# Optimization experiments

Measured on AMD Instinct MI355X. Metric: run time of the kernel, lower is better.

The kernel has to match this reference:

```python
import jax, jax.numpy as jnp
import numpy as np

N = 50000   # nodes
E = 800000  # edges
D = 128     # hidden_dim
LN_EPS = 1e-5


def _mlp2(x, W1, b1, W2, b2, act_last):
    y = jax.nn.silu(x @ W1 + b1)
    y = y @ W2 + b2
    return jax.nn.silu(y) if act_last else y


def setup_inputs() -> dict:
    key = jax.random.key(0)
    ks = jax.random.split(key, 20)
    s = 1.0 / np.sqrt(D)
    inp = {
        "h": jax.random.normal(ks[0], (N, D), jnp.float32),
        "x": jax.random.normal(ks[1], (N, 3), jnp.float32),
        "vel_all": jax.random.normal(ks[2], (N, 5, 3), jnp.float32),
        "edge_index": jax.random.randint(ks[3], (2, E), 0, N, jnp.int64),
        # phi_e: Linear(2D+11, D) -> SiLU -> Linear(D, D) -> SiLU   (weights stored [in,out])
        "We1": jax.random.uniform(ks[4], (2 * D + 11, D), jnp.float32, -s, s),
        "be1": jax.random.uniform(ks[5], (D,), jnp.float32, -s, s),
        "We2": jax.random.uniform(ks[6], (D, D), jnp.float32, -s, s),
        "be2": jax.random.uniform(ks[7], (D,), jnp.float32, -s, s),
        # phi_x: Linear(D, D) -> SiLU -> Linear(D, 1)
        "Wx1": jax.random.uniform(ks[8], (D, D), jnp.float32, -s, s),
        "bx1": jax.random.uniform(ks[9], (D,), jnp.float32, -s, s),
        "Wx2": jax.random.uniform(ks[10], (D, 1), jnp.float32, -s, s),
        "bx2": jax.random.uniform(ks[11], (1,), jnp.float32, -s, s),
        # phi_h: Linear(2D, D) -> SiLU -> Linear(D, D)
        "Wh1": jax.random.uniform(ks[12], (2 * D, D), jnp.float32, -s, s),
        "bh1": jax.random.uniform(ks[13], (D,), jnp.float32, -s, s),
        "Wh2": jax.random.uniform(ks[14], (D, D), jnp.float32, -s, s),
        "bh2": jax.random.uniform(ks[15], (D,), jnp.float32, -s, s),
        # LayerNorm(D)
        "gamma": jnp.ones((D,), jnp.float32),
        "beta": jnp.zeros((D,), jnp.float32),
    }
    return inp


def reference(h, x, vel_all, edge_index, We1, be1, We2, be2, Wx1, bx1, Wx2, bx2,
              Wh1, bh1, Wh2, bh2, gamma, beta):
    n = h.shape[0]
    src, dst = edge_index[0], edge_index[1]

    rel = x[src] - x[dst]                                  # [E,3]
    dist2 = jnp.sum(rel * rel, axis=-1, keepdims=True)     # [E,1]
    dist = jnp.maximum(jnp.sqrt(dist2), 1e-8)
    r_hat = rel / dist                                     # [E,3]

    vel_proj_src = jnp.sum(vel_all[src] * r_hat[:, None, :], axis=-1)  # [E,5]
    vel_proj_dst = jnp.sum(vel_all[dst] * r_hat[:, None, :], axis=-1)  # [E,5]

    feat = jnp.concatenate([h[src], h[dst], dist2, vel_proj_src, vel_proj_dst], axis=-1)
    m_ij = _mlp2(feat, We1, be1, We2, be2, act_last=True)  # [E,D]

    # update_coords=True: scatter_mean of rel * phi_x(m_ij)
    coord_w = _mlp2(m_ij, Wx1, bx1, Wx2, bx2, act_last=False)          # [E,1]
    num = jax.ops.segment_sum(rel * coord_w, dst, num_segments=n)      # [N,3]
    cnt = jax.ops.segment_sum(jnp.ones((rel.shape[0], 1), x.dtype), dst, num_segments=n)
    delta_x = num / jnp.maximum(cnt, 1.0)
    x = x + delta_x

    agg = jax.ops.segment_sum(m_ij, dst, num_segments=n)               # [N,D]
    dh = _mlp2(jnp.concatenate([h, agg], axis=-1), Wh1, bh1, Wh2, bh2, act_last=False)
    h = h + dh  # dropout=0 -> identity

    # LayerNorm
    mu = jnp.mean(h, axis=-1, keepdims=True)
    var = jnp.mean(jnp.square(h - mu), axis=-1, keepdims=True)
    h = (h - mu) * jax.lax.rsqrt(var + LN_EPS) * gamma + beta

    return (h, x, m_ij)
```

## Files before the change

### kernel.cpp

```cpp
#include <hip/hip_runtime.h>
#include <stdint.h>

#define CAPB 64

typedef __attribute__((ext_vector_type(8))) short bf16x8;
typedef __attribute__((ext_vector_type(4))) float f32x4;

__device__ __forceinline__ float bf2f(unsigned short u){
  union { unsigned int i; float f; } v; v.i = ((unsigned int)u) << 16; return v.f;
}
__device__ __forceinline__ unsigned short f2bf(float f){
  union { float f; unsigned int i; } v; v.f = f;
  unsigned int x = v.i;
  unsigned int r = (x + 0x7FFFu + ((x >> 16) & 1u)) >> 16;
  return (unsigned short)r;
}
__device__ __forceinline__ float silu_f(float v){
  return v / (1.0f + __expf(-v));
}

template<bool F32> __device__ __forceinline__ float ldv(const void* p, size_t i){
  if (F32) return ((const float*)p)[i];
  return bf2f(((const unsigned short*)p)[i]);
}
template<bool F32> __device__ __forceinline__ void stv(void* p, size_t i, float v){
  if (F32) ((float*)p)[i] = v;
  else     ((unsigned short*)p)[i] = f2bf(v);
}
template<bool I64> __device__ __forceinline__ int ldidx(const int* p, size_t i){
  return I64 ? p[2*i] : p[i];
}

__global__ void detect_kernel(const unsigned int* gw, const int* eidx, int N, int* flags){
  int f = 0;
  if (gw[0] == 0x3F800000u) f |= 1;
  bool i64 = true;
  for (int k = 0; k < 4; k++){
    int lo = eidx[2*k], hi = eidx[2*k+1];
    if (hi != 0 || lo < 0 || lo >= N) i64 = false;
  }
  if (i64) f |= 2;
  flags[0] = f;
}

__global__ __launch_bounds__(256) void hist_kernel(
    const int* eidx, int* cnt_i, int* bucket, int* slot, int N, int E, const int* flags)
{
  int e = blockIdx.x * 256 + threadIdx.x;
  if (e >= E) return;
  int d;
  if (flags[0] & 2) d = eidx[2*((size_t)E + e)];
  else              d = eidx[(size_t)E + e];
  d = min(max(d, 0), N-1);
  int p = atomicAdd(&cnt_i[d], 1);
  slot[e] = p;
  if (p < CAPB) bucket[(size_t)d*CAPB + p] = e;
}

struct __align__(16) NodePreSmem { float hlt[128][36]; };

template<bool F32>
__device__ void node_pre_impl(NodePreSmem& S, const void* h, const void* We1,
                              unsigned short* H1a, unsigned short* H1b, int N)
{
  const int t = threadIdx.x;
  const int base = blockIdx.x * 32;
  for (int i = t; i < 32*128; i += 256){
    int nl = i >> 7, j = i & 127;
    int node = base + nl;
    S.hlt[j][nl] = (node < N) ? ldv<F32>(h, (size_t)node*128 + j) : 0.0f;
  }
  __syncthreads();
  const int j = t & 127, half = t >> 7;
  const size_t wbase = (size_t)(half * 128) * 128;
  unsigned short* O = half ? H1b : H1a;
  float acc[32];
  #pragma unroll
  for (int nl=0; nl<32; nl++) acc[nl] = 0.0f;
  #pragma unroll 2
  for (int k=0; k<128; k++){
    float w = ldv<F32>(We1, wbase + (size_t)k*128 + j);
    const float4* row = (const float4*)&S.hlt[k][0];
    #pragma unroll
    for (int g=0; g<8; g++){
      float4 hv = row[g];
      acc[g*4+0] += hv.x * w;
      acc[g*4+1] += hv.y * w;
      acc[g*4+2] += hv.z * w;
      acc[g*4+3] += hv.w * w;
    }
  }
  #pragma unroll
  for (int nl=0; nl<32; nl++){
    int node = base + nl;
    if (node < N) O[(size_t)node*128 + j] = f2bf(acc[nl]);
  }
}

__global__ __launch_bounds__(256) void node_pre(
    const void* h, const void* We1, unsigned short* H1a, unsigned short* H1b,
    int N, const int* flags)
{
  __shared__ NodePreSmem S;
  if (flags[0] & 1) node_pre_impl<true >(S, h, We1, H1a, H1b, N);
  else              node_pre_impl<false>(S, h, We1, H1a, H1b, N);
}

template<bool F32, bool I64, bool M1F32>
__device__ void m1_impl(
    const void* xu, const void* velu, const int* eidx,
    const unsigned short* __restrict__ H1a, const unsigned short* __restrict__ H1b,
    const void* We1, const void* be1,
    void* m1p, int N, int E)
{
  const int t = threadIdx.x;
  const int sub = t & 31;
  const int j0 = sub * 4;
  float gw[11][4];
  #pragma unroll
  for (int k=0;k<11;k++)
    #pragma unroll
    for (int c=0;c<4;c++) gw[k][c] = ldv<F32>(We1, (size_t)(256+k)*128 + j0 + c);
  float b1[4];
  #pragma unroll
  for (int c=0;c<4;c++) b1[c] = ldv<F32>(be1, j0 + c);

  int gid = blockIdx.x * 8 + (t >> 5);
  const int gstride = gridDim.x * 8;
  for (int e = gid; e < E; e += gstride){
    int s = ldidx<I64>(eidx, e);
    int d = ldidx<I64>(eidx, (size_t)E + e);
    s = min(max(s, 0), N-1);
    d = min(max(d, 0), N-1);
    float rx = ldv<F32>(xu,(size_t)s*3+0) - ldv<F32>(xu,(size_t)d*3+0);
    float ry = ldv<F32>(xu,(size_t)s*3+1) - ldv<F32>(xu,(size_t)d*3+1);
    float rz = ldv<F32>(xu,(size_t)s*3+2) - ldv<F32>(xu,(size_t)d*3+2);
    float dist2 = rx*rx + ry*ry + rz*rz;
    float dist = fmaxf(sqrtf(dist2), 1e-8f);
    float inv = 1.0f / dist;
    float ux = rx*inv, uy = ry*inv, uz = rz*inv;
    float geo[11];
    geo[0] = dist2;
    #pragma unroll
    for (int v=0; v<5; v++){
      geo[1+v] = ldv<F32>(velu,(size_t)s*15+v*3+0)*ux + ldv<F32>(velu,(size_t)s*15+v*3+1)*uy + ldv<F32>(velu,(size_t)s*15+v*3+2)*uz;
      geo[6+v] = ldv<F32>(velu,(size_t)d*15+v*3+0)*ux + ldv<F32>(velu,(size_t)d*15+v*3+1)*uy + ldv<F32>(velu,(size_t)d*15+v*3+2)*uz;
    }
    uint2 ua = *(const uint2*)&H1a[(size_t)s*128 + j0];
    uint2 ub = *(const uint2*)&H1b[(size_t)d*128 + j0];
    float a[4];
    a[0] = bf2f((unsigned short)(ua.x & 0xFFFFu)) + bf2f((unsigned short)(ub.x & 0xFFFFu)) + b1[0];
    a[1] = bf2f((unsigned short)(ua.x >> 16))     + bf2f((unsigned short)(ub.x >> 16))     + b1[1];
    a[2] = bf2f((unsigned short)(ua.y & 0xFFFFu)) + bf2f((unsigned short)(ub.y & 0xFFFFu)) + b1[2];
    a[3] = bf2f((unsigned short)(ua.y >> 16))     + bf2f((unsigned short)(ub.y >> 16))     + b1[3];
    #pragma unroll
    for (int k=0;k<11;k++){
      float g = geo[k];
      #pragma unroll
      for (int c=0;c<4;c++) a[c] += gw[k][c] * g;
    }
    #pragma unroll
    for (int c=0;c<4;c++) a[c] = silu_f(a[c]);
    if (M1F32){
      float4 v = { a[0], a[1], a[2], a[3] };
      *(float4*)((float*)m1p + (size_t)e*128 + j0) = v;
    } else {
      uint2 p;
      p.x = (unsigned int)f2bf(a[0]) | ((unsigned int)f2bf(a[1]) << 16);
      p.y = (unsigned int)f2bf(a[2]) | ((unsigned int)f2bf(a[3]) << 16);
      *(uint2*)((unsigned short*)m1p + (size_t)e*128 + j0) = p;
    }
  }
}

template<bool USE_WS>
__global__ __launch_bounds__(256) void m1_kernel(
    const void* xu, const void* velu, const int* eidx,
    const unsigned short* H1a, const unsigned short* H1b,
    const void* We1, const void* be1,
    void* m1ws, void* out, size_t moff, int N, int E, const int* flags)
{
  int f = flags[0];
  if (USE_WS){
    if      (f == 0) m1_impl<false,false,false>(xu,velu,eidx,H1a,H1b,We1,be1,m1ws,N,E);
    else if (f == 1) m1_impl<true ,false,false>(xu,velu,eidx,H1a,H1b,We1,be1,m1ws,N,E);
    else if (f == 2) m1_impl<false,true ,false>(xu,velu,eidx,H1a,H1b,We1,be1,m1ws,N,E);
    else             m1_impl<true ,true ,false>(xu,velu,eidx,H1a,H1b,We1,be1,m1ws,N,E);
  } else {
    if (f & 1){
      void* p = (void*)((float*)out + moff);
      if (f & 2) m1_impl<true,true ,true>(xu,velu,eidx,H1a,H1b,We1,be1,p,N,E);
      else       m1_impl<true,false,true>(xu,velu,eidx,H1a,H1b,We1,be1,p,N,E);
    } else {
      void* p = (void*)((unsigned short*)out + moff);
      if (f & 2) m1_impl<false,true ,false>(xu,velu,eidx,H1a,H1b,We1,be1,p,N,E);
      else       m1_impl<false,false,false>(xu,velu,eidx,H1a,H1b,We1,be1,p,N,E);
    }
  }
}

struct __align__(16) GemmSmem {
  unsigned short m1s[64][136];
  unsigned short m2s[64][136];
  float relv[192];
  int   dsts[64];
  int   slot[64];
  float wpart[4][64];
};

template<bool I64>
__device__ void gemm_async_impl(GemmSmem& S,
    const float* __restrict__ xu, const int* __restrict__ eidx,
    const unsigned short* __restrict__ m1p,
    const float* __restrict__ We2, const float* __restrict__ be2,
    const float* __restrict__ Wx1, const float* __restrict__ bx1,
    const float* __restrict__ Wx2, const float* __restrict__ bx2,
    float* __restrict__ out, size_t moff,
    float* __restrict__ agg, float* __restrict__ num,
    const int* __restrict__ slotp,
    int N, int E, int ntiles)
{
  const int t = threadIdx.x;
  const int wave = t >> 6, lane = t & 63;
  const int col = lane & 15, quad = lane >> 4;
  const int colbase = wave * 32;

  bf16x8 bwe2[2][4], bwx1[2][4];
  float wx2v[2], be2v[2], bx1v[2];
  #pragma unroll
  for (int nt=0; nt<2; nt++){
    int n = colbase + nt*16 + col;
    wx2v[nt] = Wx2[n]; be2v[nt] = be2[n]; bx1v[nt] = bx1[n];
    #pragma unroll
    for (int kb=0; kb<4; kb++){
      bf16x8 a, b;
      #pragma unroll
      for (int jj=0; jj<8; jj++){
        int k = kb*32 + quad*8 + jj;
        a[jj] = (short)f2bf(We2[(size_t)k*128 + n]);
        b[jj] = (short)f2bf(Wx1[(size_t)k*128 + n]);
      }
      bwe2[nt][kb] = a; bwx1[nt][kb] = b;
    }
  }
  const float bx2v = bx2[0];
  const int srow = t >> 2, sseg = t & 3;
  const int gs = gridDim.x;

  bf16x8 r0, r1, r2, r3;
  int nsv = 0, ndv = 0, nsl = 0;
  float prx = 0, pry = 0, prz = 0;
  int pdst = 0, pvalid = 0, have_w = 0;

  int tile = blockIdx.x;
  if (tile < ntiles){
    size_t e = (size_t)tile*64 + srow; if (e >= (size_t)E) e = (size_t)E - 1;
    const unsigned short* rp = m1p + e*128 + (size_t)sseg*32;
    r0 = *(const bf16x8*)(rp);      r1 = *(const bf16x8*)(rp + 8);
    r2 = *(const bf16x8*)(rp + 16); r3 = *(const bf16x8*)(rp + 24);
    if (t < 64){
      int ec = min(tile*64 + t, E-1);
      nsv = ldidx<I64>(eidx, ec);
      ndv = ldidx<I64>(eidx, (size_t)E + ec);
      nsl = slotp[ec];
    }
  }

  for (; tile < ntiles; tile += gs){
    const int ebase = tile * 64;
    if (t < 64){
      if (have_w && pvalid){
        float w = S.wpart[0][t] + S.wpart[1][t] + S.wpart[2][t] + S.wpart[3][t] + bx2v;
        atomicAdd(&num[(size_t)pdst*3+0], prx*w);
        atomicAdd(&num[(size_t)pdst*3+1], pry*w);
        atomicAdd(&num[(size_t)pdst*3+2], prz*w);
      }
      int s = min(max(nsv, 0), N-1), d = min(max(ndv, 0), N-1);
      S.dsts[t] = d; S.slot[t] = nsl;
      pvalid = (ebase + t) < E; pdst = d;
      prx = xu[(size_t)s*3+0] - xu[(size_t)d*3+0];
      pry = xu[(size_t)s*3+1] - xu[(size_t)d*3+1];
      prz = xu[(size_t)s*3+2] - xu[(size_t)d*3+2];
    }
    *(bf16x8*)&S.m1s[srow][sseg*32 +  0] = r0;
    *(bf16x8*)&S.m1s[srow][sseg*32 +  8] = r1;
    *(bf16x8*)&S.m1s[srow][sseg*32 + 16] = r2;
    *(bf16x8*)&S.m1s[srow][sseg*32 + 24] = r3;
    if (tile + gs < ntiles){
      size_t e = (size_t)(tile+gs)*64 + srow; if (e >= (size_t)E) e = (size_t)E - 1;
      const unsigned short* rp = m1p + e*128 + (size_t)sseg*32;
      r0 = *(const bf16x8*)(rp);      r1 = *(const bf16x8*)(rp + 8);
      r2 = *(const bf16x8*)(rp + 16); r3 = *(const bf16x8*)(rp + 24);
      if (t < 64){
        int ec = min((tile+gs)*64 + t, E-1);
        nsv = ldidx<I64>(eidx, ec);
        ndv = ldidx<I64>(eidx, (size_t)E + ec);
        nsl = slotp[ec];
      }
    }
    __syncthreads();
    const int erem = E - ebase;
    #pragma unroll
    for (int et=0; et<4; et++){
      #pragma unroll
      for (int nt=0; nt<2; nt++){
        f32x4 acc = { be2v[nt], be2v[nt], be2v[nt], be2v[nt] };
        #pragma unroll
        for (int kb=0; kb<4; kb++){
          bf16x8 a = *(const bf16x8*)&S.m1s[et*16 + col][kb*32 + quad*8];
          acc = __builtin_amdgcn_mfma_f32_16x16x32_bf16(a, bwe2[nt][kb], acc, 0, 0, 0);
        }
        int n = colbase + nt*16 + col;
        #pragma unroll
        for (int r=0; r<4; r++){
          int el = et*16 + quad*4 + r;
          float v = silu_f(acc[r]);
          S.m2s[el][n] = f2bf(v);
          if (el < erem){
            out[moff + (size_t)(ebase + el)*128 + n] = v;
            if (S.slot[el] >= CAPB)
              atomicAdd(&agg[(size_t)S.dsts[el]*128 + n], v);
          }
        }
      }
    }
    __syncthreads();
    float part[4][4];
    #pragma unroll
    for (int et=0; et<4; et++)
      #pragma unroll
      for (int r=0; r<4; r++) part[et][r] = 0.0f;
    #pragma unroll
    for (int et=0; et<4; et++){
      #pragma unroll
      for (int nt=0; nt<2; nt++){
        f32x4 acc = { bx1v[nt], bx1v[nt], bx1v[nt], bx1v[nt] };
        #pragma unroll
        for (int kb=0; kb<4; kb++){
          bf16x8 a = *(const bf16x8*)&S.m2s[et*16 + col][kb*32 + quad*8];
          acc = __builtin_amdgcn_mfma_f32_16x16x32_bf16(a, bwx1[nt][kb], acc, 0, 0, 0);
        }
        #pragma unroll
        for (int r=0; r<4; r++) part[et][r] += silu_f(acc[r]) * wx2v[nt];
      }
    }
    #pragma unroll
    for (int et=0; et<4; et++){
      #pragma unroll
      for (int r=0; r<4; r++){
        float v = part[et][r];
        v += __shfl_xor(v, 1, 16);
        v += __shfl_xor(v, 2, 16);
        v += __shfl_xor(v, 4, 16);
        v += __shfl_xor(v, 8, 16);
        part[et][r] = v;
      }
    }
    if (col == 0){
      #pragma unroll
      for (int et=0; et<4; et++)
        #pragma unroll
        for (int r=0; r<4; r++)
          S.wpart[wave][et*16 + quad*4 + r] = part[et][r];
    }
    __syncthreads();
    have_w = 1;
  }
  if (t < 64 && have_w && pvalid){
    float w = S.wpart[0][t] + S.wpart[1][t] + S.wpart[2][t] + S.wpart[3][t] + bx2v;
    atomicAdd(&num[(size_t)pdst*3+0], prx*w);
    atomicAdd(&num[(size_t)pdst*3+1], pry*w);
    atomicAdd(&num[(size_t)pdst*3+2], prz*w);
  }
}

template<bool F32, bool I64, bool M1F32>
__device__ void gemm_impl(GemmSmem& S,
    const void* xu, const int* eidx, const void* m1p,
    const void* We2, const void* be2, const void* Wx1, const void* bx1,
    const void* Wx2, const void* bx2,
    void* out, size_t moff,
    float* __restrict__ agg, float* __restrict__ num,
    const int* __restrict__ slotp,
    int N, int E, int ntiles)
{
  const int t = threadIdx.x;
  const int wave = t >> 6, lane = t & 63;
  const int col = lane & 15, quad = lane >> 4;
  const int colbase = wave * 32;

  bf16x8 bwe2[2][4], bwx1[2][4];
  float wx2v[2], be2v[2], bx1v[2];
  #pragma unroll
  for (int nt=0; nt<2; nt++){
    int n = colbase + nt*16 + col;
    wx2v[nt] = ldv<F32>(Wx2, n);
    be2v[nt] = ldv<F32>(be2, n);
    bx1v[nt] = ldv<F32>(bx1, n);
    #pragma unroll
    for (int kb=0; kb<4; kb++){
      bf16x8 a, b;
      #pragma unroll
      for (int jj=0; jj<8; jj++){
        int k = kb*32 + quad*8 + jj;
        a[jj] = (short)f2bf(ldv<F32>(We2, (size_t)k*128 + n));
        b[jj] = (short)f2bf(ldv<F32>(Wx1, (size_t)k*128 + n));
      }
      bwe2[nt][kb] = a; bwx1[nt][kb] = b;
    }
  }
  const int jfix = t & 127;
  const float bx2v = ldv<F32>(bx2, 0);
  const int srow = t >> 2, sseg = t & 3;

  for (int tile = blockIdx.x; tile < ntiles; tile += gridDim.x){
    const int ebase = tile * 64;
    {
      const int e = ebase + srow;
      if (M1F32){
        const float* rp = (const float*)m1p + (size_t)e*128 + sseg*32;
        #pragma unroll
        for (int q=0;q<4;q++){
          float4 va = {0,0,0,0}, vb = {0,0,0,0};
          if (e < E){ va = *(const float4*)(rp + q*8); vb = *(const float4*)(rp + q*8 + 4); }
          bf16x8 w;
          w[0]=(short)f2bf(va.x); w[1]=(short)f2bf(va.y); w[2]=(short)f2bf(va.z); w[3]=(short)f2bf(va.w);
          w[4]=(short)f2bf(vb.x); w[5]=(short)f2bf(vb.y); w[6]=(short)f2bf(vb.z); w[7]=(short)f2bf(vb.w);
          *(bf16x8*)&S.m1s[srow][sseg*32 + q*8] = w;
        }
      } else {
        const unsigned short* rp = (const unsigned short*)m1p + (size_t)e*128 + sseg*32;
        #pragma unroll
        for (int q=0;q<4;q++){
          bf16x8 w = {0,0,0,0,0,0,0,0};
          if (e < E) w = *(const bf16x8*)(rp + q*8);
          *(bf16x8*)&S.m1s[srow][sseg*32 + q*8] = w;
        }
      }
      if (t < 64){
        int e2 = ebase + t;
        int s2 = 0, d2 = 0, sl = 0;
        if (e2 < E){
          s2 = ldidx<I64>(eidx, e2);
          d2 = ldidx<I64>(eidx, (size_t)E + e2);
          sl = slotp[e2];
        }
        s2 = min(max(s2,0), N-1); d2 = min(max(d2,0), N-1);
        S.dsts[t] = d2; S.slot[t] = sl;
        S.relv[t*3+0] = ldv<F32>(xu,(size_t)s2*3+0) - ldv<F32>(xu,(size_t)d2*3+0);
        S.relv[t*3+1] = ldv<F32>(xu,(size_t)s2*3+1) - ldv<F32>(xu,(size_t)d2*3+1);
        S.relv[t*3+2] = ldv<F32>(xu,(size_t)s2*3+2) - ldv<F32>(xu,(size_t)d2*3+2);
      }
    }
    __syncthreads();
    #pragma unroll
    for (int et=0; et<4; et++){
      #pragma unroll
      for (int nt=0; nt<2; nt++){
        f32x4 acc = { be2v[nt], be2v[nt], be2v[nt], be2v[nt] };
        #pragma unroll
        for (int kb=0; kb<4; kb++){
          bf16x8 a = *(const bf16x8*)&S.m1s[et*16 + col][kb*32 + quad*8];
          acc = __builtin_amdgcn_mfma_f32_16x16x32_bf16(a, bwe2[nt][kb], acc, 0, 0, 0);
        }
        int n = colbase + nt*16 + col;
        #pragma unroll
        for (int r=0; r<4; r++)
          S.m2s[et*16 + quad*4 + r][n] = f2bf(silu_f(acc[r]));
      }
    }
    __syncthreads();
    if (F32){
      #pragma unroll
      for (int it=0; it<4; it++){
        const int sl = t + it*256;
        const int el = sl >> 4, i8 = sl & 15;
        const int e = ebase + el;
        if (e < E){
          const bf16x8 mv = *(const bf16x8*)&S.m2s[el][i8*8];
          float f[8];
          #pragma unroll
          for (int j=0; j<8; j++) f[j] = bf2f((unsigned short)mv[j]);
          float* op = (float*)out + moff + (size_t)e*128 + i8*8;
          float4 v0 = { f[0], f[1], f[2], f[3] };
          float4 v1 = { f[4], f[5], f[6], f[7] };
          *(float4*)op = v0;
          *(float4*)(op + 4) = v1;
          if (S.slot[el] >= CAPB){
            float* ap = &agg[(size_t)S.dsts[el]*128 + i8*8];
            #pragma unroll
            for (int j=0; j<8; j++) atomicAdd(ap + j, f[j]);
          }
        }
      }
    } else {
      #pragma unroll
      for (int it=0; it<32; it++){
        int el = (t + it*256) >> 7;
        int e = ebase + el;
        if (e < E){
          float v = bf2f(S.m2s[el][jfix]);
          stv<F32>(out, moff + (size_t)e*128 + jfix, v);
          atomicAdd(&agg[(size_t)S.dsts[el]*128 + jfix], v);
        }
      }
    }
    float part[4][4];
    #pragma unroll
    for (int et=0; et<4; et++)
      #pragma unroll
      for (int r=0; r<4; r++) part[et][r] = 0.0f;
    #pragma unroll
    for (int et=0; et<4; et++){
      #pragma unroll
      for (int nt=0; nt<2; nt++){
        f32x4 acc = { bx1v[nt], bx1v[nt], bx1v[nt], bx1v[nt] };
        #pragma unroll
        for (int kb=0; kb<4; kb++){
          bf16x8 a = *(const bf16x8*)&S.m2s[et*16 + col][kb*32 + quad*8];
          acc = __builtin_amdgcn_mfma_f32_16x16x32_bf16(a, bwx1[nt][kb], acc, 0, 0, 0);
        }
        #pragma unroll
        for (int r=0; r<4; r++) part[et][r] += silu_f(acc[r]) * wx2v[nt];
      }
    }
    #pragma unroll
    for (int et=0; et<4; et++){
      #pragma unroll
      for (int r=0; r<4; r++){
        float v = part[et][r];
        v += __shfl_xor(v, 1, 16);
        v += __shfl_xor(v, 2, 16);
        v += __shfl_xor(v, 4, 16);
        v += __shfl_xor(v, 8, 16);
        part[et][r] = v;
      }
    }
    if (col == 0){
      #pragma unroll
      for (int et=0; et<4; et++)
        #pragma unroll
        for (int r=0; r<4; r++)
          S.wpart[wave][et*16 + quad*4 + r] = part[et][r];
    }
    __syncthreads();
    if (t < 64){
      int e = ebase + t;
      if (e < E){
        float w = S.wpart[0][t] + S.wpart[1][t] + S.wpart[2][t] + S.wpart[3][t] + bx2v;
        int d = S.dsts[t];
        atomicAdd(&num[(size_t)d*3+0], S.relv[t*3+0]*w);
        atomicAdd(&num[(size_t)d*3+1], S.relv[t*3+1]*w);
        atomicAdd(&num[(size_t)d*3+2], S.relv[t*3+2]*w);
      }
    }
    __syncthreads();
  }
}

template<bool USE_WS>
__global__ __launch_bounds__(256) void gemm_kernel(
    const void* xu, const int* eidx, const void* m1ws,
    const void* We2, const void* be2, const void* Wx1, const void* bx1,
    const void* Wx2, const void* bx2,
    void* out, size_t moff, float* agg, float* num, const int* slotp,
    int N, int E, int ntiles, const int* flags)
{
  __shared__ GemmSmem S;
  int f = flags[0];
  if (USE_WS && (f & 1)){
    if (f & 2) gemm_async_impl<true >(S, (const float*)xu, eidx, (const unsigned short*)m1ws,
                                      (const float*)We2,(const float*)be2,(const float*)Wx1,(const float*)bx1,
                                      (const float*)Wx2,(const float*)bx2,
                                      (float*)out, moff, agg, num, slotp, N, E, ntiles);
    else       gemm_async_impl<false>(S, (const float*)xu, eidx, (const unsigned short*)m1ws,
                                      (const float*)We2,(const float*)be2,(const float*)Wx1,(const float*)bx1,
                                      (const float*)Wx2,(const float*)bx2,
                                      (float*)out, moff, agg, num, slotp, N, E, ntiles);
  } else if (USE_WS){
    if (f & 2) gemm_impl<false,true ,false>(S, xu, eidx, m1ws, We2,be2,Wx1,bx1,Wx2,bx2, out,moff, agg,num, slotp, N,E,ntiles);
    else       gemm_impl<false,false,false>(S, xu, eidx, m1ws, We2,be2,Wx1,bx1,Wx2,bx2, out,moff, agg,num, slotp, N,E,ntiles);
  } else {
    if (f & 1){
      const void* p = (const void*)((float*)out + moff);
      if (f & 2) gemm_impl<true,true ,true>(S, xu, eidx, p, We2,be2,Wx1,bx1,Wx2,bx2, out,moff, agg,num, slotp, N,E,ntiles);
      else       gemm_impl<true,false,true>(S, xu, eidx, p, We2,be2,Wx1,bx1,Wx2,bx2, out,moff, agg,num, slotp, N,E,ntiles);
    } else {
      const void* p = (const void*)((unsigned short*)out + moff);
      if (f & 2) gemm_impl<false,true ,false>(S, xu, eidx, p, We2,be2,Wx1,bx1,Wx2,bx2, out,moff, agg,num, slotp, N,E,ntiles);
      else       gemm_impl<false,false,false>(S, xu, eidx, p, We2,be2,Wx1,bx1,Wx2,bx2, out,moff, agg,num, slotp, N,E,ntiles);
    }
  }
}

struct __align__(16) NodeFinalSmem {
  unsigned short ins[16][256];
  unsigned short y1s[16][128];
  float hns[16][128];
};

template<bool F32>
__device__ void node_final_impl(NodeFinalSmem& S,
    const void* h, const void* xu,
    const float* __restrict__ agg, const float* __restrict__ num,
    const int* __restrict__ cnt_i, const int* __restrict__ bucket,
    const void* Wh1, const void* bh1, const void* Wh2, const void* bh2,
    const void* gam, const void* bet,
    void* out, size_t xoff, size_t moff, int N)
{
  const int t = threadIdx.x;
  const int base = blockIdx.x * 16;
  for (int i = t; i < 16*128; i += 256){
    int n = i >> 7, c = i & 127;
    int node = base + n;
    S.ins[n][c] = (node < N) ? f2bf(ldv<F32>(h, (size_t)node*128 + c)) : (unsigned short)0;
  }
  if (F32){
    const int g = t >> 4, i8 = t & 15;
    const int lanebase = (t & 63) & ~15;
    const int node = base + g;
    float a[8] = {0,0,0,0,0,0,0,0};
    if (node < N){
      int deg = cnt_i[node];
      int kmax = min(deg, CAPB);
      const float* mbase = (const float*)out + moff;
      for (int c0 = 0; c0 < kmax; c0 += 16){
        int ee = 0;
        if (c0 + i8 < kmax) ee = bucket[(size_t)node*CAPB + c0 + i8];
        int cnum = min(16, kmax - c0);
        #pragma unroll
        for (int k = 0; k < 16; k++){
          if (k < cnum){
            int e = __shfl(ee, lanebase + k, 64);
            const float* rp = mbase + (size_t)e*128 + i8*8;
            float4 v0 = *(const float4*)rp;
            float4 v1 = *(const float4*)(rp + 4);
            a[0]+=v0.x; a[1]+=v0.y; a[2]+=v0.z; a[3]+=v0.w;
            a[4]+=v1.x; a[5]+=v1.y; a[6]+=v1.z; a[7]+=v1.w;
          }
        }
      }
      if (deg > CAPB){
        const float* ap = &agg[(size_t)node*128 + i8*8];
        #pragma unroll
        for (int j=0; j<8; j++) a[j] += ap[j];
      }
    }
    #pragma unroll
    for (int j=0; j<8; j++) S.ins[g][128 + i8*8 + j] = f2bf(a[j]);
  } else {
    for (int i = t; i < 16*128; i += 256){
      int n = i >> 7, c = i & 127;
      int node = base + n;
      S.ins[n][128 + c] = (node < N) ? f2bf(agg[(size_t)node*128 + c]) : (unsigned short)0;
    }
  }
  __syncthreads();
  const int j = t & 127, nh = t >> 7;
  {
    float acc[8];
    #pragma unroll
    for (int u=0; u<8; u++) acc[u] = ldv<F32>(bh1, j);
    #pragma unroll 4
    for (int k=0; k<256; k++){
      float w = ldv<F32>(Wh1, (size_t)k*128 + j);
      #pragma unroll
      for (int u=0; u<8; u++) acc[u] += bf2f(S.ins[nh + 2*u][k]) * w;
    }
    #pragma unroll
    for (int u=0; u<8; u++) S.y1s[nh + 2*u][j] = f2bf(silu_f(acc[u]));
  }
  __syncthreads();
  {
    float acc[8];
    #pragma unroll
    for (int u=0; u<8; u++) acc[u] = ldv<F32>(bh2, j);
    #pragma unroll 4
    for (int k=0; k<128; k++){
      float w = ldv<F32>(Wh2, (size_t)k*128 + j);
      #pragma unroll
      for (int u=0; u<8; u++) acc[u] += bf2f(S.y1s[nh + 2*u][k]) * w;
    }
    #pragma unroll
    for (int u=0; u<8; u++){
      int n = nh + 2*u;
      int node = base + n;
      float hv = (node < N) ? ldv<F32>(h, (size_t)node*128 + j) : 0.0f;
      S.hns[n][j] = hv + acc[u];
    }
  }
  __syncthreads();
  {
    int n = t >> 4, sub = t & 15;
    float s = 0.0f, ss = 0.0f;
    #pragma unroll
    for (int i2=0; i2<8; i2++){
      float v = S.hns[n][sub + 16*i2];
      s += v; ss += v*v;
    }
    #pragma unroll
    for (int m=1; m<16; m<<=1){ s += __shfl_xor(s, m, 16); ss += __shfl_xor(ss, m, 16); }
    float mu = s * (1.0f/128.0f);
    float var = fmaxf(ss * (1.0f/128.0f) - mu*mu, 0.0f);
    float rs = rsqrtf(var + 1e-5f);
    int gnode = base + n;
    if (gnode < N){
      #pragma unroll
      for (int i2=0; i2<8; i2++){
        int jj = sub + 16*i2;
        float v = (S.hns[n][jj] - mu) * rs * ldv<F32>(gam, jj) + ldv<F32>(bet, jj);
        stv<F32>(out, (size_t)gnode*128 + jj, v);
      }
    }
  }
  if (t < 48){
    int n = t / 3, c = t % 3;
    int node = base + n;
    if (node < N){
      float cv = fmaxf((float)cnt_i[node], 1.0f);
      float dx = num[(size_t)node*3 + c] / cv;
      stv<F32>(out, xoff + (size_t)node*3 + c, ldv<F32>(xu, (size_t)node*3 + c) + dx);
    }
  }
}

__global__ __launch_bounds__(256) void node_final(
    const void* h, const void* xu,
    const float* agg, const float* num, const int* cnt_i, const int* bucket,
    const void* Wh1, const void* bh1, const void* Wh2, const void* bh2,
    const void* gam, const void* bet,
    void* out, size_t xoff, size_t moff, int N, const int* flags)
{
  __shared__ NodeFinalSmem S;
  if (flags[0] & 1) node_final_impl<true >(S, h, xu, agg, num, cnt_i, bucket, Wh1, bh1, Wh2, bh2, gam, bet, out, xoff, moff, N);
  else              node_final_impl<false>(S, h, xu, agg, num, cnt_i, bucket, Wh1, bh1, Wh2, bh2, gam, bet, out, xoff, moff, N);
}

extern "C" void kernel_launch(void* const* d_in, const int* in_sizes, int n_in,
                              void* d_out, int out_size, void* d_ws, size_t ws_size,
                              hipStream_t stream)
{
  const int N = in_sizes[0] / 128;
  const int E = in_sizes[3] / 2;

  char* ws = (char*)d_ws;
  int* flags = (int*)ws;
  size_t off = 256;
  unsigned short* H1a = (unsigned short*)(ws + off); off += (size_t)N*256;
  unsigned short* H1b = (unsigned short*)(ws + off); off += (size_t)N*256;
  float* agg   = (float*)(ws + off); off += (size_t)N*512;
  float* num   = (float*)(ws + off); off += (size_t)N*12;
  int*   cnt_i = (int*)(ws + off); off += (size_t)N*4;
  int*   bucket= (int*)(ws + off); off += (size_t)N*CAPB*4;
  int*   slot  = (int*)(ws + off); off += (size_t)E*4;
  void*  m1ws  = (void*)(ws + off); off += (size_t)E*256;
  const bool use_ws = (off <= ws_size);

  detect_kernel<<<1, 1, 0, stream>>>((const unsigned int*)d_in[16], (const int*)d_in[3], N, flags);

  size_t zbytes = (size_t)N*512 + (size_t)N*12 + (size_t)N*4;
  hipMemsetAsync((void*)agg, 0, zbytes, stream);

  hist_kernel<<<(E + 255) / 256, 256, 0, stream>>>((const int*)d_in[3], cnt_i, bucket, slot, N, E, flags);

  node_pre<<<(N + 31) / 32, 256, 0, stream>>>(d_in[0], d_in[4], H1a, H1b, N, flags);

  size_t xoff = (size_t)N * 128;
  size_t moff = (size_t)N * 128 + (size_t)N * 3;
  int ntiles = (E + 63) / 64;

  if (use_ws){
    m1_kernel<true><<<2048, 256, 0, stream>>>(d_in[1], d_in[2], (const int*)d_in[3], H1a, H1b,
                                              d_in[4], d_in[5], m1ws, d_out, moff, N, E, flags);
    gemm_kernel<true><<<2500, 256, 0, stream>>>(d_in[1], (const int*)d_in[3], m1ws,
                                                d_in[6], d_in[7], d_in[8], d_in[9],
                                                d_in[10], d_in[11],
                                                d_out, moff, agg, num, slot, N, E, ntiles, flags);
  } else {
    m1_kernel<false><<<2048, 256, 0, stream>>>(d_in[1], d_in[2], (const int*)d_in[3], H1a, H1b,
                                               d_in[4], d_in[5], m1ws, d_out, moff, N, E, flags);
    gemm_kernel<false><<<2500, 256, 0, stream>>>(d_in[1], (const int*)d_in[3], m1ws,
                                                 d_in[6], d_in[7], d_in[8], d_in[9],
                                                 d_in[10], d_in[11],
                                                 d_out, moff, agg, num, slot, N, E, ntiles, flags);
  }

  node_final<<<(N + 15) / 16, 256, 0, stream>>>(d_in[0], d_in[1], agg, num, cnt_i, bucket,
                                                d_in[12], d_in[13], d_in[14], d_in[15],
                                                d_in[16], d_in[17],
                                                d_out, xoff, moff, N, flags);
}
```

Before: 1.356 ms.

## Sort edges by destination via counting sort and segment-reduce aggregation in GEMM

Builds a destination-sorted edge permutation using histogram, a single-block prefix scan, and a scatter kernel. The edge MLP kernels then process edges in sorted order. The GEMM kernel reduces runs of equal destinations before issuing atomic adds to agg, and stores m_ij back to the original edge positions through the permutation. This removes the per-node bucket gather in the node kernel and the capped-bucket scheme. In exchange it adds extra launches including a serial single-block scan, scattered output writes, and the loss of the previous register prefetch pipeline in the GEMM kernel.

```diff
diff --git a/kernel.cpp b/kernel.cpp
--- a/kernel.cpp
+++ b/kernel.cpp
@@ -1,7 +1,5 @@
 #include <hip/hip_runtime.h>
 #include <stdint.h>
-
-#define CAPB 64
 
 typedef __attribute__((ext_vector_type(8))) short bf16x8;
 typedef __attribute__((ext_vector_type(4))) float f32x4;
@@ -44,7 +42,7 @@
 }
 
 __global__ __launch_bounds__(256) void hist_kernel(
-    const int* eidx, int* cnt_i, int* bucket, int* slot, int N, int E, const int* flags)
+    const int* eidx, int* cnt_i, int* slot, int N, int E, const int* flags)
 {
   int e = blockIdx.x * 256 + threadIdx.x;
   if (e >= E) return;
@@ -54,7 +52,47 @@
   d = min(max(d, 0), N-1);
   int p = atomicAdd(&cnt_i[d], 1);
   slot[e] = p;
-  if (p < CAPB) bucket[(size_t)d*CAPB + p] = e;
+}
+
+__global__ __launch_bounds__(256) void scan_kernel(const int* __restrict__ cnt_i, int* __restrict__ start, int N){
+  __shared__ int wsum[4];
+  const int t = threadIdx.x;
+  const int lane = t & 63, w = t >> 6;
+  int total = 0;
+  for (int base = 0; base < N; base += 256){
+    int i = base + t;
+    int v = (i < N) ? cnt_i[i] : 0;
+    int orig = v;
+    #pragma unroll
+    for (int off = 1; off < 64; off <<= 1){
+      int u = __shfl_up(v, off, 64);
+      if (lane >= off) v += u;
+    }
+    if (lane == 63) wsum[w] = v;
+    __syncthreads();
+    int wpre = 0;
+    #pragma unroll
+    for (int k = 0; k < 4; k++){
+      if (k < w) wpre += wsum[k];
+    }
+    int chunk_total = wsum[0] + wsum[1] + wsum[2] + wsum[3];
+    if (i < N) start[i] = total + wpre + (v - orig);
+    total += chunk_total;
+    __syncthreads();
+  }
+}
+
+__global__ __launch_bounds__(256) void perm_build(
+    const int* eidx, const int* slot, const int* start,
+    int* perm, int* dstp, int N, int E, const int* flags)
+{
+  int e = blockIdx.x * 256 + threadIdx.x;
+  if (e >= E) return;
+  int d = (flags[0] & 2) ? eidx[2*((size_t)E + e)] : eidx[(size_t)E + e];
+  d = min(max(d, 0), N-1);
+  int pos = start[d] + slot[e];
+  perm[pos] = e;
+  dstp[pos] = d;
 }
 
 struct __align__(16) NodePreSmem { float hlt[128][36]; };
@@ -106,12 +144,13 @@
   else              node_pre_impl<false>(S, h, We1, H1a, H1b, N);
 }
 
-template<bool F32, bool I64, bool M1F32>
+template<bool F32, bool I64, bool M1F32, bool PERM>
 __device__ void m1_impl(
     const void* xu, const void* velu, const int* eidx,
     const unsigned short* __restrict__ H1a, const unsigned short* __restrict__ H1b,
     const void* We1, const void* be1,
-    void* m1p, int N, int E)
+    void* m1p, const int* __restrict__ permp, float* __restrict__ relp,
+    int N, int E)
 {
   const int t = threadIdx.x;
   const int sub = t & 31;
@@ -127,7 +166,8 @@
 
   int gid = blockIdx.x * 8 + (t >> 5);
   const int gstride = gridDim.x * 8;
-  for (int e = gid; e < E; e += gstride){
+  for (int pos = gid; pos < E; pos += gstride){
+    const int e = PERM ? permp[pos] : pos;
     int s = ldidx<I64>(eidx, e);
     int d = ldidx<I64>(eidx, (size_t)E + e);
     s = min(max(s, 0), N-1);
@@ -146,6 +186,11 @@
       geo[1+v] = ldv<F32>(velu,(size_t)s*15+v*3+0)*ux + ldv<F32>(velu,(size_t)s*15+v*3+1)*uy + ldv<F32>(velu,(size_t)s*15+v*3+2)*uz;
       geo[6+v] = ldv<F32>(velu,(size_t)d*15+v*3+0)*ux + ldv<F32>(velu,(size_t)d*15+v*3+1)*uy + ldv<F32>(velu,(size_t)d*15+v*3+2)*uz;
     }
+    if (PERM){
+      if (sub == 0) relp[(size_t)pos*3 + 0] = rx;
+      if (sub == 1) relp[(size_t)pos*3 + 1] = ry;
+      if (sub == 2) relp[(size_t)pos*3 + 2] = rz;
+    }
     uint2 ua = *(const uint2*)&H1a[(size_t)s*128 + j0];
     uint2 ub = *(const uint2*)&H1b[(size_t)d*128 + j0];
     float a[4];
@@ -163,12 +208,12 @@
     for (int c=0;c<4;c++) a[c] = silu_f(a[c]);
     if (M1F32){
       float4 v = { a[0], a[1], a[2], a[3] };
-      *(float4*)((float*)m1p + (size_t)e*128 + j0) = v;
+      *(float4*)((float*)m1p + (size_t)pos*128 + j0) = v;
     } else {
       uint2 p;
       p.x = (unsigned int)f2bf(a[0]) | ((unsigned int)f2bf(a[1]) << 16);
       p.y = (unsigned int)f2bf(a[2]) | ((unsigned int)f2bf(a[3]) << 16);
-      *(uint2*)((unsigned short*)m1p + (size_t)e*128 + j0) = p;
+      *(uint2*)((unsigned short*)m1p + (size_t)pos*128 + j0) = p;
     }
   }
 }
@@ -178,23 +223,24 @@
     const void* xu, const void* velu, const int* eidx,
     const unsigned short* H1a, const unsigned short* H1b,
     const void* We1, const void* be1,
-    void* m1ws, void* out, size_t moff, int N, int E, const int* flags)
+    void* m1ws, void* out, size_t moff, const int* perm, float* relp,
+    int N, int E, const int* flags)
 {
   int f = flags[0];
   if (USE_WS){
-    if      (f == 0) m1_impl<false,false,false>(xu,velu,eidx,H1a,H1b,We1,be1,m1ws,N,E);
-    else if (f == 1) m1_impl<true ,false,false>(xu,velu,eidx,H1a,H1b,We1,be1,m1ws,N,E);
-    else if (f == 2) m1_impl<false,true ,false>(xu,velu,eidx,H1a,H1b,We1,be1,m1ws,N,E);
-    else             m1_impl<true ,true ,false>(xu,velu,eidx,H1a,H1b,We1,be1,m1ws,N,E);
+    if      (f == 0) m1_impl<false,false,false,false>(xu,velu,eidx,H1a,H1b,We1,be1,m1ws,perm,relp,N,E);
+    else if (f == 1) m1_impl<true ,false,false,true >(xu,velu,eidx,H1a,H1b,We1,be1,m1ws,perm,relp,N,E);
+    else if (f == 2) m1_impl<false,true ,false,false>(xu,velu,eidx,H1a,H1b,We1,be1,m1ws,perm,relp,N,E);
+    else             m1_impl<true ,true ,false,true >(xu,velu,eidx,H1a,H1b,We1,be1,m1ws,perm,relp,N,E);
   } else {
     if (f & 1){
       void* p = (void*)((float*)out + moff);
-      if (f & 2) m1_impl<true,true ,true>(xu,velu,eidx,H1a,H1b,We1,be1,p,N,E);
-      else       m1_impl<true,false,true>(xu,velu,eidx,H1a,H1b,We1,be1,p,N,E);
+      if (f & 2) m1_impl<true,true ,true,false>(xu,velu,eidx,H1a,H1b,We1,be1,p,perm,relp,N,E);
+      else       m1_impl<true,false,true,false>(xu,velu,eidx,H1a,H1b,We1,be1,p,perm,relp,N,E);
     } else {
       void* p = (void*)((unsigned short*)out + moff);
-      if (f & 2) m1_impl<false,true ,false>(xu,velu,eidx,H1a,H1b,We1,be1,p,N,E);
-      else       m1_impl<false,false,false>(xu,velu,eidx,H1a,H1b,We1,be1,p,N,E);
+      if (f & 2) m1_impl<false,true ,false,false>(xu,velu,eidx,H1a,H1b,We1,be1,p,perm,relp,N,E);
+      else       m1_impl<false,false,false,false>(xu,velu,eidx,H1a,H1b,We1,be1,p,perm,relp,N,E);
     }
   }
 }
@@ -208,16 +254,25 @@
   float wpart[4][64];
 };
 
-template<bool I64>
-__device__ void gemm_async_impl(GemmSmem& S,
-    const float* __restrict__ xu, const int* __restrict__ eidx,
+struct __align__(16) GemmPermSmem {
+  unsigned short m1s[64][136];
+  unsigned short m2s[64][136];
+  float relv[192];
+  int   dstrow[64];
+  int   outp[64];
+  float wpart[4][64];
+};
+
+union GemmSmemU { GemmSmem a; GemmPermSmem b; };
+
+__device__ void gemm_perm_impl(GemmPermSmem& S,
     const unsigned short* __restrict__ m1p,
+    const int* __restrict__ perm, const int* __restrict__ dstp, const float* __restrict__ relp,
     const float* __restrict__ We2, const float* __restrict__ be2,
     const float* __restrict__ Wx1, const float* __restrict__ bx1,
     const float* __restrict__ Wx2, const float* __restrict__ bx2,
     float* __restrict__ out, size_t moff,
     float* __restrict__ agg, float* __restrict__ num,
-    const int* __restrict__ slotp,
     int N, int E, int ntiles)
 {
   const int t = threadIdx.x;
@@ -245,61 +300,30 @@
   }
   const float bx2v = bx2[0];
   const int srow = t >> 2, sseg = t & 3;
-  const int gs = gridDim.x;
-
-  bf16x8 r0, r1, r2, r3;
-  int nsv = 0, ndv = 0, nsl = 0;
-  float prx = 0, pry = 0, prz = 0;
-  int pdst = 0, pvalid = 0, have_w = 0;
-
-  int tile = blockIdx.x;
-  if (tile < ntiles){
-    size_t e = (size_t)tile*64 + srow; if (e >= (size_t)E) e = (size_t)E - 1;
-    const unsigned short* rp = m1p + e*128 + (size_t)sseg*32;
-    r0 = *(const bf16x8*)(rp);      r1 = *(const bf16x8*)(rp + 8);
-    r2 = *(const bf16x8*)(rp + 16); r3 = *(const bf16x8*)(rp + 24);
-    if (t < 64){
-      int ec = min(tile*64 + t, E-1);
-      nsv = ldidx<I64>(eidx, ec);
-      ndv = ldidx<I64>(eidx, (size_t)E + ec);
-      nsl = slotp[ec];
-    }
-  }
-
-  for (; tile < ntiles; tile += gs){
+
+  for (int tile = blockIdx.x; tile < ntiles; tile += gridDim.x){
     const int ebase = tile * 64;
-    if (t < 64){
-      if (have_w && pvalid){
-        float w = S.wpart[0][t] + S.wpart[1][t] + S.wpart[2][t] + S.wpart[3][t] + bx2v;
-        atomicAdd(&num[(size_t)pdst*3+0], prx*w);
-        atomicAdd(&num[(size_t)pdst*3+1], pry*w);
-        atomicAdd(&num[(size_t)pdst*3+2], prz*w);
-      }
-      int s = min(max(nsv, 0), N-1), d = min(max(ndv, 0), N-1);
-      S.dsts[t] = d; S.slot[t] = nsl;
-      pvalid = (ebase + t) < E; pdst = d;
-      prx = xu[(size_t)s*3+0] - xu[(size_t)d*3+0];
-      pry = xu[(size_t)s*3+1] - xu[(size_t)d*3+1];
-      prz = xu[(size_t)s*3+2] - xu[(size_t)d*3+2];
-    }
-    *(bf16x8*)&S.m1s[srow][sseg*32 +  0] = r0;
-    *(bf16x8*)&S.m1s[srow][sseg*32 +  8] = r1;
-    *(bf16x8*)&S.m1s[srow][sseg*32 + 16] = r2;
-    *(bf16x8*)&S.m1s[srow][sseg*32 + 24] = r3;
-    if (tile + gs < ntiles){
-      size_t e = (size_t)(tile+gs)*64 + srow; if (e >= (size_t)E) e = (size_t)E - 1;
-      const unsigned short* rp = m1p + e*128 + (size_t)sseg*32;
-      r0 = *(const bf16x8*)(rp);      r1 = *(const bf16x8*)(rp + 8);
-      r2 = *(const bf16x8*)(rp + 16); r3 = *(const bf16x8*)(rp + 24);
+    {
+      const int p = ebase + srow;
+      const unsigned short* rp = m1p + (size_t)p*128 + sseg*32;
+      #pragma unroll
+      for (int q=0;q<4;q++){
+        bf16x8 w = {0,0,0,0,0,0,0,0};
+        if (p < E) w = *(const bf16x8*)(rp + q*8);
+        *(bf16x8*)&S.m1s[srow][sseg*32 + q*8] = w;
+      }
       if (t < 64){
-        int ec = min((tile+gs)*64 + t, E-1);
-        nsv = ldidx<I64>(eidx, ec);
-        ndv = ldidx<I64>(eidx, (size_t)E + ec);
-        nsl = slotp[ec];
-      }
-    }
-    __syncthreads();
-    const int erem = E - ebase;
+        int pp = ebase + t;
+        bool val = pp < E;
+        S.outp[t]   = val ? perm[pp] : 0;
+        S.dstrow[t] = val ? dstp[pp] : -1;
+      }
+      if (t < 192){
+        int p3 = ebase*3 + t;
+        S.relv[t] = (p3 < E*3) ? relp[p3] : 0.0f;
+      }
+    }
+    __syncthreads();
     #pragma unroll
     for (int et=0; et<4; et++){
       #pragma unroll
@@ -312,19 +336,43 @@
         }
         int n = colbase + nt*16 + col;
         #pragma unroll
-        for (int r=0; r<4; r++){
-          int el = et*16 + quad*4 + r;
-          float v = silu_f(acc[r]);
-          S.m2s[el][n] = f2bf(v);
-          if (el < erem){
-            out[moff + (size_t)(ebase + el)*128 + n] = v;
-            if (S.slot[el] >= CAPB)
-              atomicAdd(&agg[(size_t)S.dsts[el]*128 + n], v);
-          }
-        }
-      }
-    }
-    __syncthreads();
+        for (int r=0; r<4; r++)
+          S.m2s[et*16 + quad*4 + r][n] = f2bf(silu_f(acc[r]));
+      }
+    }
+    __syncthreads();
+    #pragma unroll
+    for (int it=0; it<4; it++){
+      const int sl = t + it*256;
+      const int el = sl >> 4, i8 = sl & 15;
+      if (ebase + el < E){
+        const bf16x8 mv = *(const bf16x8*)&S.m2s[el][i8*8];
+        float f[8];
+        #pragma unroll
+        for (int j=0; j<8; j++) f[j] = bf2f((unsigned short)mv[j]);
+        float* op = out + moff + (size_t)S.outp[el]*128 + i8*8;
+        float4 v0 = { f[0], f[1], f[2], f[3] };
+        float4 v1 = { f[4], f[5], f[6], f[7] };
+        *(float4*)op = v0;
+        *(float4*)(op + 4) = v1;
+      }
+    }
+    {
+      const int j = t & 127, half = t >> 7;
+      float run = 0.0f; int cur = -1;
+      #pragma unroll 4
+      for (int r=0; r<32; r++){
+        int g = half*32 + r;
+        int d = S.dstrow[g];
+        float v = bf2f(S.m2s[g][j]);
+        if (d != cur){
+          if (cur >= 0) atomicAdd(&agg[(size_t)cur*128 + j], run);
+          run = 0.0f; cur = d;
+        }
+        run += v;
+      }
+      if (cur >= 0) atomicAdd(&agg[(size_t)cur*128 + j], run);
+    }
     float part[4][4];
     #pragma unroll
     for (int et=0; et<4; et++)
@@ -364,13 +412,16 @@
           S.wpart[wave][et*16 + quad*4 + r] = part[et][r];
     }
     __syncthreads();
-    have_w = 1;
-  }
-  if (t < 64 && have_w && pvalid){
-    float w = S.wpart[0][t] + S.wpart[1][t] + S.wpart[2][t] + S.wpart[3][t] + bx2v;
-    atomicAdd(&num[(size_t)pdst*3+0], prx*w);
-    atomicAdd(&num[(size_t)pdst*3+1], pry*w);
-    atomicAdd(&num[(size_t)pdst*3+2], prz*w);
+    if (t < 64){
+      if (ebase + t < E){
+        float w = S.wpart[0][t] + S.wpart[1][t] + S.wpart[2][t] + S.wpart[3][t] + bx2v;
+        int d = S.dstrow[t];
+        atomicAdd(&num[(size_t)d*3+0], S.relv[t*3+0]*w);
+        atomicAdd(&num[(size_t)d*3+1], S.relv[t*3+1]*w);
+        atomicAdd(&num[(size_t)d*3+2], S.relv[t*3+2]*w);
+      }
+    }
+    __syncthreads();
   }
 }
 
@@ -381,7 +432,6 @@
     const void* Wx2, const void* bx2,
     void* out, size_t moff,
     float* __restrict__ agg, float* __restrict__ num,
-    const int* __restrict__ slotp,
     int N, int E, int ntiles)
 {
   const int t = threadIdx.x;
@@ -439,14 +489,13 @@
       }
       if (t < 64){
         int e2 = ebase + t;
-        int s2 = 0, d2 = 0, sl = 0;
+        int s2 = 0, d2 = 0;
         if (e2 < E){
           s2 = ldidx<I64>(eidx, e2);
           d2 = ldidx<I64>(eidx, (size_t)E + e2);
-          sl = slotp[e2];
         }
         s2 = min(max(s2,0), N-1); d2 = min(max(d2,0), N-1);
-        S.dsts[t] = d2; S.slot[t] = sl;
+        S.dsts[t] = d2;
         S.relv[t*3+0] = ldv<F32>(xu,(size_t)s2*3+0) - ldv<F32>(xu,(size_t)d2*3+0);
         S.relv[t*3+1] = ldv<F32>(xu,(size_t)s2*3+1) - ldv<F32>(xu,(size_t)d2*3+1);
         S.relv[t*3+2] = ldv<F32>(xu,(size_t)s2*3+2) - ldv<F32>(xu,(size_t)d2*3+2);
@@ -486,11 +535,9 @@
           float4 v1 = { f[4], f[5], f[6], f[7] };
           *(float4*)op = v0;
           *(float4*)(op + 4) = v1;
-          if (S.slot[el] >= CAPB){
-            float* ap = &agg[(size_t)S.dsts[el]*128 + i8*8];
-            #pragma unroll
-            for (int j=0; j<8; j++) atomicAdd(ap + j, f[j]);
-          }
+          float* ap = &agg[(size_t)S.dsts[el]*128 + i8*8];
+          #pragma unroll
+          for (int j=0; j<8; j++) atomicAdd(ap + j, f[j]);
         }
       }
     } else {
@@ -561,34 +608,31 @@
 template<bool USE_WS>
 __global__ __launch_bounds__(256) void gemm_kernel(
     const void* xu, const int* eidx, const void* m1ws,
+    const int* perm, const int* dstp, const float* relp,
     const void* We2, const void* be2, const void* Wx1, const void* bx1,
     const void* Wx2, const void* bx2,
-    void* out, size_t moff, float* agg, float* num, const int* slotp,
+    void* out, size_t moff, float* agg, float* num,
     int N, int E, int ntiles, const int* flags)
 {
-  __shared__ GemmSmem S;
+  __shared__ GemmSmemU U;
   int f = flags[0];
   if (USE_WS && (f & 1)){
-    if (f & 2) gemm_async_impl<true >(S, (const float*)xu, eidx, (const unsigned short*)m1ws,
-                                      (const float*)We2,(const float*)be2,(const float*)Wx1,(const float*)bx1,
-                                      (const float*)Wx2,(const float*)bx2,
-                                      (float*)out, moff, agg, num, slotp, N, E, ntiles);
-    else       gemm_async_impl<false>(S, (const float*)xu, eidx, (const unsigned short*)m1ws,
-                                      (const float*)We2,(const float*)be2,(const float*)Wx1,(const float*)bx1,
-                                      (const float*)Wx2,(const float*)bx2,
-                                      (float*)out, moff, agg, num, slotp, N, E, ntiles);
+    gemm_perm_impl(U.b, (const unsigned short*)m1ws, perm, dstp, relp,
+                   (const float*)We2,(const float*)be2,(const float*)Wx1,(const float*)bx1,
+                   (const float*)Wx2,(const float*)bx2,
+                   (float*)out, moff, agg, num, N, E, ntiles);
   } else if (USE_WS){
-    if (f & 2) gemm_impl<false,true ,false>(S, xu, eidx, m1ws, We2,be2,Wx1,bx1,Wx2,bx2, out,moff, agg,num, slotp, N,E,ntiles);
-    else       gemm_impl<false,false,false>(S, xu, eidx, m1ws, We2,be2,Wx1,bx1,Wx2,bx2, out,moff, agg,num, slotp, N,E,ntiles);
+    if (f & 2) gemm_impl<false,true ,false>(U.a, xu, eidx, m1ws, We2,be2,Wx1,bx1,Wx2,bx2, out,moff, agg,num, N,E,ntiles);
+    else       gemm_impl<false,false,false>(U.a, xu, eidx, m1ws, We2,be2,Wx1,bx1,Wx2,bx2, out,moff, agg,num, N,E,ntiles);
   } else {
     if (f & 1){
       const void* p = (const void*)((float*)out + moff);
-      if (f & 2) gemm_impl<true,true ,true>(S, xu, eidx, p, We2,be2,Wx1,bx1,Wx2,bx2, out,moff, agg,num, slotp, N,E,ntiles);
-      else       gemm_impl<true,false,true>(S, xu, eidx, p, We2,be2,Wx1,bx1,Wx2,bx2, out,moff, agg,num, slotp, N,E,ntiles);
+      if (f & 2) gemm_impl<true,true ,true>(U.a, xu, eidx, p, We2,be2,Wx1,bx1,Wx2,bx2, out,moff, agg,num, N,E,ntiles);
+      else       gemm_impl<true,false,true>(U.a, xu, eidx, p, We2,be2,Wx1,bx1,Wx2,bx2, out,moff, agg,num, N,E,ntiles);
     } else {
       const void* p = (const void*)((unsigned short*)out + moff);
-      if (f & 2) gemm_impl<false,true ,false>(S, xu, eidx, p, We2,be2,Wx1,bx1,Wx2,bx2, out,moff, agg,num, slotp, N,E,ntiles);
-      else       gemm_impl<false,false,false>(S, xu, eidx, p, We2,be2,Wx1,bx1,Wx2,bx2, out,moff, agg,num, slotp, N,E,ntiles);
+      if (f & 2) gemm_impl<false,true ,false>(U.a, xu, eidx, p, We2,be2,Wx1,bx1,Wx2,bx2, out,moff, agg,num, N,E,ntiles);
+      else       gemm_impl<false,false,false>(U.a, xu, eidx, p, We2,be2,Wx1,bx1,Wx2,bx2, out,moff, agg,num, N,E,ntiles);
     }
   }
 }
@@ -603,57 +647,18 @@
 __device__ void node_final_impl(NodeFinalSmem& S,
     const void* h, const void* xu,
     const float* __restrict__ agg, const float* __restrict__ num,
-    const int* __restrict__ cnt_i, const int* __restrict__ bucket,
+    const int* __restrict__ cnt_i,
     const void* Wh1, const void* bh1, const void* Wh2, const void* bh2,
     const void* gam, const void* bet,
-    void* out, size_t xoff, size_t moff, int N)
+    void* out, size_t xoff, int N)
 {
   const int t = threadIdx.x;
   const int base = blockIdx.x * 16;
   for (int i = t; i < 16*128; i += 256){
     int n = i >> 7, c = i & 127;
     int node = base + n;
-    S.ins[n][c] = (node < N) ? f2bf(ldv<F32>(h, (size_t)node*128 + c)) : (unsigned short)0;
-  }
-  if (F32){
-    const int g = t >> 4, i8 = t & 15;
-    const int lanebase = (t & 63) & ~15;
-    const int node = base + g;
-    float a[8] = {0,0,0,0,0,0,0,0};
-    if (node < N){
-      int deg = cnt_i[node];
-      int kmax = min(deg, CAPB);
-      const float* mbase = (const float*)out + moff;
-      for (int c0 = 0; c0 < kmax; c0 += 16){
-        int ee = 0;
-        if (c0 + i8 < kmax) ee = bucket[(size_t)node*CAPB + c0 + i8];
-        int cnum = min(16, kmax - c0);
-        #pragma unroll
-        for (int k = 0; k < 16; k++){
-          if (k < cnum){
-            int e = __shfl(ee, lanebase + k, 64);
-            const float* rp = mbase + (size_t)e*128 + i8*8;
-            float4 v0 = *(const float4*)rp;
-            float4 v1 = *(const float4*)(rp + 4);
-            a[0]+=v0.x; a[1]+=v0.y; a[2]+=v0.z; a[3]+=v0.w;
-            a[4]+=v1.x; a[5]+=v1.y; a[6]+=v1.z; a[7]+=v1.w;
-          }
-        }
-      }
-      if (deg > CAPB){
-        const float* ap = &agg[(size_t)node*128 + i8*8];
-        #pragma unroll
-        for (int j=0; j<8; j++) a[j] += ap[j];
-      }
-    }
-    #pragma unroll
-    for (int j=0; j<8; j++) S.ins[g][128 + i8*8 + j] = f2bf(a[j]);
-  } else {
-    for (int i = t; i < 16*128; i += 256){
-      int n = i >> 7, c = i & 127;
-      int node = base + n;
-      S.ins[n][128 + c] = (node < N) ? f2bf(agg[(size_t)node*128 + c]) : (unsigned short)0;
-    }
+    S.ins[n][c]       = (node < N) ? f2bf(ldv<F32>(h, (size_t)node*128 + c)) : (unsigned short)0;
+    S.ins[n][128 + c] = (node < N) ? f2bf(agg[(size_t)node*128 + c])         : (unsigned short)0;
   }
   __syncthreads();
   const int j = t & 127, nh = t >> 7;
@@ -726,14 +731,14 @@
 
 __global__ __launch_bounds__(256) void node_final(
     const void* h, const void* xu,
-    const float* agg, const float* num, const int* cnt_i, const int* bucket,
+    const float* agg, const float* num, const int* cnt_i,
     const void* Wh1, const void* bh1, const void* Wh2, const void* bh2,
     const void* gam, const void* bet,
-    void* out, size_t xoff, size_t moff, int N, const int* flags)
+    void* out, size_t xoff, int N, const int* flags)
 {
   __shared__ NodeFinalSmem S;
-  if (flags[0] & 1) node_final_impl<true >(S, h, xu, agg, num, cnt_i, bucket, Wh1, bh1, Wh2, bh2, gam, bet, out, xoff, moff, N);
-  else              node_final_impl<false>(S, h, xu, agg, num, cnt_i, bucket, Wh1, bh1, Wh2, bh2, gam, bet, out, xoff, moff, N);
+  if (flags[0] & 1) node_final_impl<true >(S, h, xu, agg, num, cnt_i, Wh1, bh1, Wh2, bh2, gam, bet, out, xoff, N);
+  else              node_final_impl<false>(S, h, xu, agg, num, cnt_i, Wh1, bh1, Wh2, bh2, gam, bet, out, xoff, N);
 }
 
 extern "C" void kernel_launch(void* const* d_in, const int* in_sizes, int n_in,
@@ -751,8 +756,11 @@
   float* agg   = (float*)(ws + off); off += (size_t)N*512;
   float* num   = (float*)(ws + off); off += (size_t)N*12;
   int*   cnt_i = (int*)(ws + off); off += (size_t)N*4;
-  int*   bucket= (int*)(ws + off); off += (size_t)N*CAPB*4;
-  int*   slot  = (int*)(ws + off); off += (size_t)E*4;
+  int*   start = (int*)(ws + off); off += (size_t)(N+64)*4;
+  int*   perm  = (int*)(ws + off); off += (size_t)E*4;
+  int*   dstp  = (int*)(ws + off); off += (size_t)E*4;
+  float* relp  = (float*)(ws + off); off += (size_t)E*12;
+  int*   slot  = (int*)relp;
   void*  m1ws  = (void*)(ws + off); off += (size_t)E*256;
   const bool use_ws = (off <= ws_size);
 
@@ -761,7 +769,9 @@
   size_t zbytes = (size_t)N*512 + (size_t)N*12 + (size_t)N*4;
   hipMemsetAsync((void*)agg, 0, zbytes, stream);
 
-  hist_kernel<<<(E + 255) / 256, 256, 0, stream>>>((const int*)d_in[3], cnt_i, bucket, slot, N, E, flags);
+  hist_kernel<<<(E + 255) / 256, 256, 0, stream>>>((const int*)d_in[3], cnt_i, slot, N, E, flags);
+  scan_kernel<<<1, 256, 0, stream>>>(cnt_i, start, N);
+  perm_build<<<(E + 255) / 256, 256, 0, stream>>>((const int*)d_in[3], slot, start, perm, dstp, N, E, flags);
 
   node_pre<<<(N + 31) / 32, 256, 0, stream>>>(d_in[0], d_in[4], H1a, H1b, N, flags);
 
@@ -771,22 +781,22 @@
 
   if (use_ws){
     m1_kernel<true><<<2048, 256, 0, stream>>>(d_in[1], d_in[2], (const int*)d_in[3], H1a, H1b,
-                                              d_in[4], d_in[5], m1ws, d_out, moff, N, E, flags);
-    gemm_kernel<true><<<2500, 256, 0, stream>>>(d_in[1], (const int*)d_in[3], m1ws,
+                                              d_in[4], d_in[5], m1ws, d_out, moff, perm, relp, N, E, flags);
+    gemm_kernel<true><<<2500, 256, 0, stream>>>(d_in[1], (const int*)d_in[3], m1ws, perm, dstp, relp,
                                                 d_in[6], d_in[7], d_in[8], d_in[9],
                                                 d_in[10], d_in[11],
-                                                d_out, moff, agg, num, slot, N, E, ntiles, flags);
+                                                d_out, moff, agg, num, N, E, ntiles, flags);
   } else {
     m1_kernel<false><<<2048, 256, 0, stream>>>(d_in[1], d_in[2], (const int*)d_in[3], H1a, H1b,
-                                               d_in[4], d_in[5], m1ws, d_out, moff, N, E, flags);
-    gemm_kernel<false><<<2500, 256, 0, stream>>>(d_in[1], (const int*)d_in[3], m1ws,
+                                               d_in[4], d_in[5], m1ws, d_out, moff, perm, relp, N, E, flags);
+    gemm_kernel<false><<<2500, 256, 0, stream>>>(d_in[1], (const int*)d_in[3], m1ws, perm, dstp, relp,
                                                  d_in[6], d_in[7], d_in[8], d_in[9],
                                                  d_in[10], d_in[11],
-                                                 d_out, moff, agg, num, slot, N, E, ntiles, flags);
-  }
-
-  node_final<<<(N + 15) / 16, 256, 0, stream>>>(d_in[0], d_in[1], agg, num, cnt_i, bucket,
+                                                 d_out, moff, agg, num, N, E, ntiles, flags);
+  }
+
+  node_final<<<(N + 15) / 16, 256, 0, stream>>>(d_in[0], d_in[1], agg, num, cnt_i,
                                                 d_in[12], d_in[13], d_in[14], d_in[15],
                                                 d_in[16], d_in[17],
-                                                d_out, xoff, moff, N, flags);
-}
+                                                d_out, xoff, N, flags);
+}
```

Measured after the change: 1.564 ms. 1.15x slower.
